# Kernel optimization log

Measured on AMD Instinct MI355X. Metric: run time of the kernel, lower is better.

Reference implementation:

```python
import jax, jax.numpy as jnp
import numpy as np

B, T, C, H = 2, 2048, 1024, 16
HD = C // H  # head dim = 64


def setup_inputs() -> dict:
    key = jax.random.key(0)
    k1, k2, k3 = jax.random.split(key, 3)
    scale_in = 1.0 / np.sqrt(C)
    x = jax.random.normal(k1, (B, T, C), dtype=jnp.float32)
    w_qkv = jax.random.normal(k2, (C, 3 * C), dtype=jnp.float32) * scale_in
    b_qkv = jnp.zeros((3 * C,), dtype=jnp.float32)
    w_out = jax.random.normal(k3, (C, C), dtype=jnp.float32) * scale_in
    b_out = jnp.zeros((C,), dtype=jnp.float32)
    return {"x": x, "w_qkv": w_qkv, "b_qkv": b_qkv, "w_out": w_out, "b_out": b_out}


def reference(x, w_qkv, b_qkv, w_out, b_out):
    Bq, Tq, Cq = x.shape
    qkv = x @ w_qkv + b_qkv                       # [B,T,3C]
    q, k, v = jnp.split(qkv, 3, axis=-1)          # each [B,T,C]
    # [B,T,C] -> [B,H,T,HD]
    q = q.reshape(Bq, Tq, H, HD).transpose(0, 2, 1, 3)
    k = k.reshape(Bq, Tq, H, HD).transpose(0, 2, 1, 3)
    v = v.reshape(Bq, Tq, H, HD).transpose(0, 2, 1, 3)
    scale = 1.0 / np.sqrt(HD)
    scores = jnp.einsum("bhqd,bhkd->bhqk", q, k) * scale  # [B,H,T,T]
    causal = jnp.tril(jnp.ones((Tq, Tq), dtype=bool))
    scores = jnp.where(causal[None, None], scores, jnp.finfo(scores.dtype).min)
    attn = jax.nn.softmax(scores, axis=-1)
    y = jnp.einsum("bhqk,bhkd->bhqd", attn, v)    # [B,H,T,HD]
    y = y.transpose(0, 2, 1, 3).reshape(Bq, Tq, Cq)
    return y @ w_out + b_out
```

## Files before the change

kernel.cpp:

```cpp
#include <hip/hip_runtime.h>
#include <hip/hip_bf16.h>


#define B_ 2
#define T_ 2048
#define C_ 1024
#define H_ 16
#define HD_ 64
#define M_ (B_ * T_)
#define N3_ (3 * C_)
#define QK2_ 2048
#define QSCALE 0.18033688f

typedef __attribute__((ext_vector_type(8))) short short8;
typedef __attribute__((ext_vector_type(4))) short short4v;
typedef __attribute__((ext_vector_type(4))) float floatx4;

__device__ __forceinline__ unsigned short f2b(float f) {
    __hip_bfloat16 h = __float2bfloat16(f);
    return *reinterpret_cast<unsigned short*>(&h);
}

__device__ __forceinline__ void glds16(const void* g, void* l) {
    __builtin_amdgcn_global_load_lds(
        (const __attribute__((address_space(1))) void*)g,
        (__attribute__((address_space(3))) void*)l, 16, 0, 0);
}

__global__ __launch_bounds__(256) void pack_bf16(
    const float* __restrict__ src, unsigned short* __restrict__ dst) {
    int i = (blockIdx.x * 256 + threadIdx.x) * 4;
    float4 v = *reinterpret_cast<const float4*>(src + i);
    short4v s;
    s[0] = (short)f2b(v.x); s[1] = (short)f2b(v.y);
    s[2] = (short)f2b(v.z); s[3] = (short)f2b(v.w);
    *reinterpret_cast<short4v*>(dst + i) = s;
}

__global__ __launch_bounds__(256) void transpose_pack(
    const float* __restrict__ src, unsigned short* __restrict__ dst,
    int K, int N) {
    __shared__ float t[32][33];
    const int n0 = blockIdx.x * 32, k0 = blockIdx.y * 32;
    const int tx = threadIdx.x & 31, ty = threadIdx.x >> 5;
#pragma unroll
    for (int i = 0; i < 4; i++)
        t[ty + i * 8][tx] = src[(size_t)(k0 + ty + i * 8) * N + n0 + tx];
    __syncthreads();
#pragma unroll
    for (int i = 0; i < 4; i++)
        dst[(size_t)(n0 + ty + i * 8) * K + k0 + tx] = f2b(t[tx][ty + i * 8]);
}

template<int EPI, int BN>
__global__ __launch_bounds__(256) void gemm_glds(
    const unsigned short* __restrict__ A, const unsigned short* __restrict__ Bt,
    const float* __restrict__ bias, void* __restrict__ Cp,
    unsigned short* __restrict__ vtp, int M, int N, int K) {
    constexpr int NI = BN / 32;
    __shared__ __align__(16) unsigned short Al[128 * 32];
    __shared__ __align__(16) unsigned short Bl[BN * 32];

    const int tid  = threadIdx.x;
    const int lane = tid & 63;
    const int w    = tid >> 6;
    const int c16  = lane & 15;
    const int quad = lane >> 4;
    const int n0 = blockIdx.x * BN;
    const int m0 = blockIdx.y * 128;
    const int wm = (w >> 1) * 64;
    const int wn = (w & 1) * (BN / 2);

    floatx4 acc[4][NI] = {};

    const int srow = w * 32 + (lane >> 2);
    const int scol = (lane & 3) * 8;
    const unsigned short* ag = A + (size_t)(m0 + srow) * K + scol;
    unsigned short* al0 = &Al[(w * 32) * 32];
    unsigned short* al1 = &Al[(w * 32 + 16) * 32];
    const int srowB = w * (BN / 4) + (lane >> 2);
    const unsigned short* bg = Bt + (size_t)(n0 + srowB) * K + scol;

    for (int k0 = 0; k0 < K; k0 += 32) {
        __syncthreads();
        glds16(ag + k0, al0);
        glds16(ag + k0 + (size_t)16 * K, al1);
#pragma unroll
        for (int i = 0; i < BN / 64; i++)
            glds16(bg + k0 + (size_t)(i * 16) * K,
                   &Bl[(w * (BN / 4) + i * 16) * 32]);
        __syncthreads();

        short8 af[4], bf[NI];
#pragma unroll
        for (int im = 0; im < 4; im++)
            af[im] = *reinterpret_cast<const short8*>(
                &Al[(wm + im * 16 + c16) * 32 + quad * 8]);
#pragma unroll
        for (int in = 0; in < NI; in++)
            bf[in] = *reinterpret_cast<const short8*>(
                &Bl[(wn + in * 16 + c16) * 32 + quad * 8]);
#pragma unroll
        for (int im = 0; im < 4; im++)
#pragma unroll
            for (int in = 0; in < NI; in++)
                acc[im][in] = __builtin_amdgcn_mfma_f32_16x16x32_bf16(
                    af[im], bf[in], acc[im][in], 0, 0, 0);
    }

    const int ncol = n0 + wn;
    float bv[NI];
#pragma unroll
    for (int in = 0; in < NI; in++) bv[in] = bias[ncol + in * 16 + c16];

    if (EPI == 0) {
        float* C = (float*)Cp;
#pragma unroll
        for (int im = 0; im < 4; im++)
#pragma unroll
            for (int r = 0; r < 4; r++) {
                int row = m0 + wm + im * 16 + quad * 4 + r;
#pragma unroll
                for (int in = 0; in < NI; in++)
                    C[(size_t)row * N + ncol + in * 16 + c16] =
                        acc[im][in][r] + bv[in];
            }
    } else {
        if (ncol < 2 * C_) {
            const float fac = (ncol < C_) ? QSCALE : 1.0f;
            unsigned short* qkp = (unsigned short*)Cp;
#pragma unroll
            for (int im = 0; im < 4; im++)
#pragma unroll
                for (int r = 0; r < 4; r++) {
                    int row = m0 + wm + im * 16 + quad * 4 + r;
#pragma unroll
                    for (int in = 0; in < NI; in++)
                        qkp[(size_t)row * QK2_ + ncol + in * 16 + c16] =
                            f2b((acc[im][in][r] + bv[in]) * fac);
                }
        } else {
#pragma unroll
            for (int im = 0; im < 4; im++) {
                int row0 = m0 + wm + im * 16 + quad * 4;
                int b  = row0 >> 11;
                int t0 = row0 & (T_ - 1);
#pragma unroll
                for (int in = 0; in < NI; in++) {
                    int dfull = ncol - 2 * C_ + in * 16 + c16;
                    short4v sv;
#pragma unroll
                    for (int r = 0; r < 4; r++)
                        sv[r] = (short)f2b(acc[im][in][r] + bv[in]);
                    *reinterpret_cast<short4v*>(
                        &vtp[(((size_t)(b << 10) + dfull) << 11) + t0]) = sv;
                }
            }
        }
    }
}

__device__ __forceinline__ void attn_tile(
    short8 af0, short8 af1,
    const unsigned short* __restrict__ Kl,
    const unsigned short* __restrict__ Vl,
    unsigned short* __restrict__ pw,
    floatx4 O[4], float lrow[4],
    int row0, int kb, int c16, int quad) {
    const floatx4 z = {0.f, 0.f, 0.f, 0.f};
    const int sx  = c16 & 7;
    const int ch0 = (quad ^ sx) * 8;
    const int ch1 = ((quad + 4) ^ sx) * 8;
    floatx4 s[4];
#pragma unroll
    for (int nt = 0; nt < 4; nt++) {
        const int rb = (nt * 16 + c16) * 64;
        short8 k0 = *reinterpret_cast<const short8*>(&Kl[rb + ch0]);
        short8 k1 = *reinterpret_cast<const short8*>(&Kl[rb + ch1]);
        floatx4 t = __builtin_amdgcn_mfma_f32_16x16x32_bf16(af0, k0, z, 0, 0, 0);
        s[nt] = __builtin_amdgcn_mfma_f32_16x16x32_bf16(af1, k1, t, 0, 0, 0);
    }
#pragma unroll
    for (int nt = 0; nt < 4; nt++)
#pragma unroll
        for (int r = 0; r < 4; r++) {
            int key = kb + nt * 16 + c16;
            int row = row0 + quad * 4 + r;
            float p = (key <= row) ? exp2f(s[nt][r]) : 0.f;
            lrow[r] += p;
            pw[(quad * 4 + r) * 72 + nt * 16 + c16] = f2b(p);
        }
    short8 pf0 = *reinterpret_cast<const short8*>(&pw[c16 * 72 + quad * 8]);
    short8 pf1 = *reinterpret_cast<const short8*>(&pw[c16 * 72 + 32 + quad * 8]);
#pragma unroll
    for (int nt = 0; nt < 4; nt++) {
        const int rb = (nt * 16 + c16) * 64;
        short8 v0 = *reinterpret_cast<const short8*>(&Vl[rb + ch0]);
        short8 v1 = *reinterpret_cast<const short8*>(&Vl[rb + ch1]);
        floatx4 t = __builtin_amdgcn_mfma_f32_16x16x32_bf16(pf0, v0, O[nt], 0, 0, 0);
        O[nt] = __builtin_amdgcn_mfma_f32_16x16x32_bf16(pf1, v1, t, 0, 0, 0);
    }
}

__global__ __launch_bounds__(256) void attn_mfma(
    const unsigned short* __restrict__ qk,
    const unsigned short* __restrict__ vt,
    unsigned short* __restrict__ y) {
    __shared__ __align__(16) unsigned short Kl[64 * 64];
    __shared__ __align__(16) unsigned short Vl[64 * 64];
    __shared__ __align__(16) unsigned short Pl[4 * 16 * 72];

    const int tid  = threadIdx.x;
    const int lane = tid & 63;
    const int w    = tid >> 6;
    const int c16  = lane & 15;
    const int quad = lane >> 4;
    const int bh = blockIdx.x & 31;
    const int t  = 31 - (blockIdx.x >> 5);
    const int b  = bh >> 4;
    const int h  = bh & 15;
    const int row0 = (4 * t + w) * 16;
    const int nch  = t + 1;

    const unsigned short* qrow = qk + (size_t)b * T_ * QK2_ + h * HD_;
    const unsigned short* krow = qrow + C_;
    const unsigned short* vrow = vt + ((size_t)bh << 6) * T_;

    short8 af0 = *reinterpret_cast<const short8*>(
        qrow + (size_t)(row0 + c16) * QK2_ + quad * 8);
    short8 af1 = *reinterpret_cast<const short8*>(
        qrow + (size_t)(row0 + c16) * QK2_ + 32 + quad * 8);

    floatx4 O[4] = {};
    float lrow[4] = {};
    unsigned short* pw = &Pl[w * 16 * 72];

    const int r8 = lane >> 3;
    const int sw = ((lane & 7) ^ r8) * 8;

    for (int c = 0; c < nch; c++) {
        const int kb = c * 64;
        __syncthreads();
#pragma unroll
        for (int i = 0; i < 2; i++) {
            const int row = w * 16 + i * 8 + r8;
            glds16(krow + (size_t)(kb + row) * QK2_ + sw,
                   &Kl[(w * 16 + i * 8) * 64]);
            glds16(vrow + (size_t)row * T_ + kb + sw,
                   &Vl[(w * 16 + i * 8) * 64]);
        }
        __syncthreads();

        attn_tile(af0, af1, Kl, Vl, pw, O, lrow, row0, kb, c16, quad);
    }

#pragma unroll
    for (int r = 0; r < 4; r++)
#pragma unroll
        for (int off = 1; off < 16; off <<= 1)
            lrow[r] += __shfl_xor(lrow[r], off);

#pragma unroll
    for (int nt = 0; nt < 4; nt++)
#pragma unroll
        for (int r = 0; r < 4; r++) {
            float val = O[nt][r] / fmaxf(lrow[r], 1e-30f);
            y[((size_t)b * T_ + row0 + quad * 4 + r) * C_ + h * HD_ + nt * 16 + c16] =
                f2b(val);
        }
}

extern "C" void kernel_launch(void* const* d_in, const int* in_sizes, int n_in,
                              void* d_out, int out_size, void* d_ws, size_t ws_size,
                              hipStream_t stream) {
    const float* x     = (const float*)d_in[0];
    const float* w_qkv = (const float*)d_in[1];
    const float* b_qkv = (const float*)d_in[2];
    const float* w_out = (const float*)d_in[3];
    const float* b_out = (const float*)d_in[4];
    float* out = (float*)d_out;

    unsigned short* qkb = (unsigned short*)d_ws;
    unsigned short* vtb = qkb + (size_t)M_ * QK2_;
    unsigned short* yb  = vtb + (size_t)B_ * H_ * HD_ * T_;
    unsigned short* wt1 = yb + (size_t)M_ * C_;
    unsigned short* wt2 = wt1 + (size_t)N3_ * C_;
    unsigned short* xb  = wt2 + (size_t)C_ * C_;

    pack_bf16<<<M_ * C_ / 1024, 256, 0, stream>>>(x, xb);
    transpose_pack<<<dim3(N3_ / 32, C_ / 32), 256, 0, stream>>>(w_qkv, wt1, C_, N3_);
    transpose_pack<<<dim3(C_ / 32, C_ / 32), 256, 0, stream>>>(w_out, wt2, C_, C_);

    dim3 g1(N3_ / 128, M_ / 128);
    gemm_glds<1, 128><<<g1, 256, 0, stream>>>(xb, wt1, b_qkv, qkb, vtb, M_, N3_, C_);

    attn_mfma<<<B_ * H_ * 32, 256, 0, stream>>>(qkb, vtb, yb);

    dim3 g2(C_ / 64, M_ / 128);
    gemm_glds<0, 64><<<g2, 256, 0, stream>>>(yb, wt2, b_out, out, nullptr, M_, C_, C_);
}
```

Baseline: 192.3 us.

## Double GEMM K-tile with swizzled LDS; skip masking on full attention tiles

The GEMM now stages a K-slab of 64 instead of 32 per iteration, using an XOR-swizzled LDS layout so the wider rows avoid bank conflicts. This halves the barrier and load-issue count per K and doubles the MFMAs issued per sync. The attention kernel swaps the MFMA operands so each lane holds one query row. That allows vectorized short4 writes of P and a single row-sum reduction with fewer shuffles. The causal mask is applied only on the final diagonal tile. The cost is larger LDS per GEMM block, which may reduce occupancy.

```diff
diff --git a/kernel.cpp b/kernel.cpp
--- a/kernel.cpp
+++ b/kernel.cpp
@@ -58,8 +58,8 @@
     const float* __restrict__ bias, void* __restrict__ Cp,
     unsigned short* __restrict__ vtp, int M, int N, int K) {
     constexpr int NI = BN / 32;
-    __shared__ __align__(16) unsigned short Al[128 * 32];
-    __shared__ __align__(16) unsigned short Bl[BN * 32];
+    __shared__ __align__(16) unsigned short Al[128 * 64];
+    __shared__ __align__(16) unsigned short Bl[BN * 64];
 
     const int tid  = threadIdx.x;
     const int lane = tid & 63;
@@ -73,39 +73,45 @@
 
     floatx4 acc[4][NI] = {};
 
-    const int srow = w * 32 + (lane >> 2);
-    const int scol = (lane & 3) * 8;
-    const unsigned short* ag = A + (size_t)(m0 + srow) * K + scol;
-    unsigned short* al0 = &Al[(w * 32) * 32];
-    unsigned short* al1 = &Al[(w * 32 + 16) * 32];
-    const int srowB = w * (BN / 4) + (lane >> 2);
-    const unsigned short* bg = Bt + (size_t)(n0 + srowB) * K + scol;
-
-    for (int k0 = 0; k0 < K; k0 += 32) {
+    const int srow = lane >> 3;
+    const int sch  = ((lane & 7) ^ srow) * 8;
+    const unsigned short* ag = A + (size_t)(m0 + w * 32 + srow) * K + sch;
+    const unsigned short* bg = Bt + (size_t)(n0 + w * (BN / 4) + srow) * K + sch;
+
+    const int s7 = c16 & 7;
+
+    for (int k0 = 0; k0 < K; k0 += 64) {
         __syncthreads();
-        glds16(ag + k0, al0);
-        glds16(ag + k0 + (size_t)16 * K, al1);
-#pragma unroll
-        for (int i = 0; i < BN / 64; i++)
-            glds16(bg + k0 + (size_t)(i * 16) * K,
-                   &Bl[(w * (BN / 4) + i * 16) * 32]);
+#pragma unroll
+        for (int i = 0; i < 4; i++)
+            glds16(ag + k0 + (size_t)(i * 8) * K, &Al[(w * 32 + i * 8) * 64]);
+#pragma unroll
+        for (int i = 0; i < BN / 32; i++)
+            glds16(bg + k0 + (size_t)(i * 8) * K,
+                   &Bl[(w * (BN / 4) + i * 8) * 64]);
         __syncthreads();
 
-        short8 af[4], bf[NI];
+        short8 af[4][2], bf[NI][2];
 #pragma unroll
         for (int im = 0; im < 4; im++)
-            af[im] = *reinterpret_cast<const short8*>(
-                &Al[(wm + im * 16 + c16) * 32 + quad * 8]);
+#pragma unroll
+            for (int kk = 0; kk < 2; kk++)
+                af[im][kk] = *reinterpret_cast<const short8*>(
+                    &Al[(wm + im * 16 + c16) * 64 + ((kk * 4 + quad) ^ s7) * 8]);
 #pragma unroll
         for (int in = 0; in < NI; in++)
-            bf[in] = *reinterpret_cast<const short8*>(
-                &Bl[(wn + in * 16 + c16) * 32 + quad * 8]);
+#pragma unroll
+            for (int kk = 0; kk < 2; kk++)
+                bf[in][kk] = *reinterpret_cast<const short8*>(
+                    &Bl[(wn + in * 16 + c16) * 64 + ((kk * 4 + quad) ^ s7) * 8]);
 #pragma unroll
         for (int im = 0; im < 4; im++)
 #pragma unroll
             for (int in = 0; in < NI; in++)
-                acc[im][in] = __builtin_amdgcn_mfma_f32_16x16x32_bf16(
-                    af[im], bf[in], acc[im][in], 0, 0, 0);
+#pragma unroll
+                for (int kk = 0; kk < 2; kk++)
+                    acc[im][in] = __builtin_amdgcn_mfma_f32_16x16x32_bf16(
+                        af[im][kk], bf[in][kk], acc[im][in], 0, 0, 0);
     }
 
     const int ncol = n0 + wn;
@@ -160,12 +166,13 @@
     }
 }
 
+template<bool MASKED>
 __device__ __forceinline__ void attn_tile(
     short8 af0, short8 af1,
     const unsigned short* __restrict__ Kl,
     const unsigned short* __restrict__ Vl,
     unsigned short* __restrict__ pw,
-    floatx4 O[4], float lrow[4],
+    floatx4 O[4], float& l,
     int row0, int kb, int c16, int quad) {
     const floatx4 z = {0.f, 0.f, 0.f, 0.f};
     const int sx  = c16 & 7;
@@ -177,19 +184,27 @@
         const int rb = (nt * 16 + c16) * 64;
         short8 k0 = *reinterpret_cast<const short8*>(&Kl[rb + ch0]);
         short8 k1 = *reinterpret_cast<const short8*>(&Kl[rb + ch1]);
-        floatx4 t = __builtin_amdgcn_mfma_f32_16x16x32_bf16(af0, k0, z, 0, 0, 0);
-        s[nt] = __builtin_amdgcn_mfma_f32_16x16x32_bf16(af1, k1, t, 0, 0, 0);
-    }
-#pragma unroll
-    for (int nt = 0; nt < 4; nt++)
+        floatx4 t = __builtin_amdgcn_mfma_f32_16x16x32_bf16(k0, af0, z, 0, 0, 0);
+        s[nt] = __builtin_amdgcn_mfma_f32_16x16x32_bf16(k1, af1, t, 0, 0, 0);
+    }
+    const int qrow = row0 + c16;
+#pragma unroll
+    for (int nt = 0; nt < 4; nt++) {
+        short4v p4;
 #pragma unroll
         for (int r = 0; r < 4; r++) {
-            int key = kb + nt * 16 + c16;
-            int row = row0 + quad * 4 + r;
-            float p = (key <= row) ? exp2f(s[nt][r]) : 0.f;
-            lrow[r] += p;
-            pw[(quad * 4 + r) * 72 + nt * 16 + c16] = f2b(p);
+            float p;
+            if (MASKED) {
+                int key = kb + nt * 16 + quad * 4 + r;
+                p = (key <= qrow) ? exp2f(s[nt][r]) : 0.f;
+            } else {
+                p = exp2f(s[nt][r]);
+            }
+            l += p;
+            p4[r] = (short)f2b(p);
         }
+        *reinterpret_cast<short4v*>(&pw[c16 * 72 + nt * 16 + quad * 4]) = p4;
+    }
     short8 pf0 = *reinterpret_cast<const short8*>(&pw[c16 * 72 + quad * 8]);
     short8 pf1 = *reinterpret_cast<const short8*>(&pw[c16 * 72 + 32 + quad * 8]);
 #pragma unroll
@@ -232,7 +247,7 @@
         qrow + (size_t)(row0 + c16) * QK2_ + 32 + quad * 8);
 
     floatx4 O[4] = {};
-    float lrow[4] = {};
+    float l = 0.f;
     unsigned short* pw = &Pl[w * 16 * 72];
 
     const int r8 = lane >> 3;
@@ -251,20 +266,24 @@
         }
         __syncthreads();
 
-        attn_tile(af0, af1, Kl, Vl, pw, O, lrow, row0, kb, c16, quad);
-    }
-
+        if (c + 1 < nch)
+            attn_tile<false>(af0, af1, Kl, Vl, pw, O, l, row0, kb, c16, quad);
+        else
+            attn_tile<true>(af0, af1, Kl, Vl, pw, O, l, row0, kb, c16, quad);
+    }
+
+    l += __shfl_xor(l, 16);
+    l += __shfl_xor(l, 32);
+    float lr[4];
 #pragma unroll
     for (int r = 0; r < 4; r++)
-#pragma unroll
-        for (int off = 1; off < 16; off <<= 1)
-            lrow[r] += __shfl_xor(lrow[r], off);
+        lr[r] = __shfl(l, quad * 4 + r);
 
 #pragma unroll
     for (int nt = 0; nt < 4; nt++)
 #pragma unroll
         for (int r = 0; r < 4; r++) {
-            float val = O[nt][r] / fmaxf(lrow[r], 1e-30f);
+            float val = O[nt][r] / fmaxf(lr[r], 1e-30f);
             y[((size_t)b * T_ + row0 + quad * 4 + r) * C_ + h * HD_ + nt * 16 + c16] =
                 f2b(val);
         }
```

Result: faster. 180.0 us (-6.4%).
